# Optimization experiments

Hardware: AMD Instinct MI355X
Metric: run time of the kernel (lower is better)

## Reference

```python
import jax, jax.numpy as jnp
import numpy as np

N_NODES = 50000
N_EDGES = 800000
NFEAT, NHID, NCLASS = 512, 128, 16


def _with_self_loops(edge_idx, n):
    loop = jnp.arange(n, dtype=edge_idx.dtype)
    src = jnp.concatenate([edge_idx[0], loop])  # [E+N]
    dst = jnp.concatenate([edge_idx[1], loop])
    return src, dst


def gcn_conv(x, src, dst, W, b, n):
    # GCNConv with add aggregation, self-loops, symmetric normalization.
    h = x @ W  # [N, out]
    ones = jnp.ones(src.shape[0], dtype=h.dtype)
    deg = jax.ops.segment_sum(ones, dst, num_segments=n)  # in-degree incl. self-loops
    dinv = jnp.where(deg > 0, jax.lax.rsqrt(deg), 0.0)
    norm = dinv[src] * dinv[dst]  # [E+N]
    msg = h[src] * norm[:, None]  # gather + scale
    out = jax.ops.segment_sum(msg, dst, num_segments=n)  # scatter-add
    return out + b


def setup_inputs() -> dict:
    key = jax.random.key(0)
    ks = jax.random.split(key, 8)
    x = jax.random.normal(ks[0], (N_NODES, NFEAT), dtype=jnp.float32)
    edge_idx = jax.random.randint(ks[1], (2, N_EDGES), 0, N_NODES, dtype=jnp.int64)
    s1 = 1.0 / np.sqrt(NFEAT)
    s2 = 1.0 / np.sqrt(NHID)
    W1 = jax.random.uniform(ks[2], (NFEAT, NHID), jnp.float32, -s1, s1)
    b1 = jnp.zeros((NHID,), jnp.float32)
    W2 = jax.random.uniform(ks[3], (NHID, NHID), jnp.float32, -s2, s2)
    b2 = jnp.zeros((NHID,), jnp.float32)
    Wc = jax.random.uniform(ks[4], (NHID, NCLASS), jnp.float32, -s2, s2)
    bc = jax.random.uniform(ks[5], (NCLASS,), jnp.float32, -s2, s2)
    return {"x": x, "edge_idx": edge_idx, "W1": W1, "b1": b1, "W2": W2, "b2": b2, "Wc": Wc, "bc": bc}


def reference(x, edge_idx, W1, b1, W2, b2, Wc, bc):
    n = x.shape[0]
    src, dst = _with_self_loops(edge_idx, n)
    h = gcn_conv(x, src, dst, W1, b1, n)
    h = jax.nn.relu(h)  # dropout is identity in eval mode
    h = gcn_conv(h, src, dst, W2, b2, n)
    h = jax.nn.relu(h)
    logits = h @ Wc + bc
    return jax.nn.log_softmax(logits, axis=1)
```

## Files before the change

### kernel.cpp

```cpp
#include <hip/hip_runtime.h>
#include <math.h>

#define NFEAT 512
#define NHID  128
#define NCLASS 16
#define SCAN_BS 512

typedef __attribute__((ext_vector_type(8))) short short8;
typedef __attribute__((ext_vector_type(4))) float f32x4;

static __device__ __forceinline__ ushort f2b(float f) {
    union { float f; uint u; } v; v.f = f;
    uint r = v.u + 0x7FFFu + ((v.u >> 16) & 1u);
    return (ushort)(r >> 16);
}
static __device__ __forceinline__ float b2f(uint bits) {
    union { uint u; float f; } v; v.u = bits << 16; return v.f;
}


__global__ void k_init_deg(int* __restrict__ deg, int n) {
    int i = blockIdx.x * blockDim.x + threadIdx.x;
    if (i < n) deg[i] = 1;
}

__global__ void k_count(const int* __restrict__ dst, int e, int* __restrict__ deg) {
    int i = blockIdx.x * blockDim.x + threadIdx.x;
    if (i < e) atomicAdd(&deg[dst[i]], 1);
}

__global__ void k_dinv(const int* __restrict__ deg, float* __restrict__ dinv,
                       int* __restrict__ cursor, int n) {
    int i = blockIdx.x * blockDim.x + threadIdx.x;
    if (i < n) {
        dinv[i] = rsqrtf((float)deg[i]);
        cursor[i] = 0;
    }
}

__global__ void k_scan1(const int* __restrict__ deg, int* __restrict__ offs,
                        int* __restrict__ bsum, int n) {
    __shared__ int s[SCAN_BS];
    int t = threadIdx.x;
    int i = blockIdx.x * SCAN_BS + t;
    int v = (i < n) ? deg[i] : 0;
    s[t] = v;
    for (int off = 1; off < SCAN_BS; off <<= 1) {
        __syncthreads();
        int x = (t >= off) ? s[t - off] : 0;
        __syncthreads();
        s[t] += x;
    }
    __syncthreads();
    if (i < n) offs[i] = s[t] - v;
    if (t == SCAN_BS - 1) bsum[blockIdx.x] = s[t];
}

__global__ void k_scan2(int* __restrict__ bsum, int* __restrict__ offs, int nb, int n) {
    if (threadIdx.x == 0 && blockIdx.x == 0) {
        int run = 0;
        for (int b = 0; b < nb; b++) { int x = bsum[b]; bsum[b] = run; run += x; }
        offs[n] = run;
    }
}

__global__ void k_scan3(int* __restrict__ offs, const int* __restrict__ bsum, int n) {
    int i = blockIdx.x * SCAN_BS + threadIdx.x;
    if (i < n) offs[i] += bsum[blockIdx.x];
}

__global__ void k_fill_edges(const int* __restrict__ src, const int* __restrict__ dst, int e,
                             const int* __restrict__ offs, int* __restrict__ cursor,
                             int* __restrict__ col) {
    int i = blockIdx.x * blockDim.x + threadIdx.x;
    if (i < e) {
        int d = dst[i];
        int p = atomicAdd(&cursor[d], 1);
        col[offs[d] + p] = src[i];
    }
}

__global__ void k_fill_self(const int* __restrict__ offs, int* __restrict__ cursor,
                            int* __restrict__ col, int n) {
    int i = blockIdx.x * blockDim.x + threadIdx.x;
    if (i < n) {
        int p = atomicAdd(&cursor[i], 1);
        col[offs[i] + p] = i;
    }
}


__global__ void k_tcast(const float* __restrict__ W, ushort* __restrict__ WT, int K) {
    int idx = blockIdx.x * 256 + threadIdx.x;
    if (idx < K * 128) {
        int k = idx >> 7, c = idx & 127;
        WT[(size_t)c * K + k] = f2b(W[idx]);
    }
}


template<int A_F32>
__global__ __launch_bounds__(256) void k_gemm(const void* __restrict__ Aptr,
                                              const ushort* __restrict__ WT,
                                              const float* __restrict__ rowscale,
                                              ushort* __restrict__ H, int M, int K) {
    __shared__ ushort As[128][40];
    __shared__ ushort Bs[128][40];

    const int tid = threadIdx.x;
    const int wid = tid >> 6, lane = tid & 63;
    const int wr = wid >> 1, wc = wid & 1;
    const int lr = lane & 15, lk = (lane >> 4) * 8;
    const int rowbase = blockIdx.x * 128;

    f32x4 acc[4][4];
#pragma unroll
    for (int i = 0; i < 4; i++)
#pragma unroll
        for (int j = 0; j < 4; j++) acc[i][j] = (f32x4)0.f;

    const int sr = tid >> 1;
    const int sh = (tid & 1) * 16;

    for (int k0 = 0; k0 < K; k0 += 32) {
        {
            int gr = rowbase + sr;
            ushort tmp[16];
            if (A_F32) {
                const float* A = (const float*)Aptr;
                if (gr < M) {
                    const float* p = A + (size_t)gr * K + k0 + sh;
#pragma unroll
                    for (int q = 0; q < 4; q++) {
                        float4 v = *(const float4*)(p + q * 4);
                        tmp[q * 4 + 0] = f2b(v.x); tmp[q * 4 + 1] = f2b(v.y);
                        tmp[q * 4 + 2] = f2b(v.z); tmp[q * 4 + 3] = f2b(v.w);
                    }
                } else {
#pragma unroll
                    for (int q = 0; q < 16; q++) tmp[q] = 0;
                }
            } else {
                const ushort* A = (const ushort*)Aptr;
                if (gr < M) {
                    const ushort* p = A + (size_t)gr * K + k0 + sh;
                    *(short8*)&tmp[0] = *(const short8*)(p);
                    *(short8*)&tmp[8] = *(const short8*)(p + 8);
                } else {
#pragma unroll
                    for (int q = 0; q < 16; q++) tmp[q] = 0;
                }
            }
            *(short8*)&As[sr][sh]     = *(short8*)&tmp[0];
            *(short8*)&As[sr][sh + 8] = *(short8*)&tmp[8];
        }
        {
#pragma unroll
            for (int t = 0; t < 2; t++) {
                int c = tid + t * 256;
                int row = c >> 2, q = c & 3;
                short8 v = *(const short8*)(WT + (size_t)row * K + k0 + q * 8);
                *(short8*)&Bs[row][q * 8] = v;
            }
        }
        __syncthreads();

        short8 af[4], bfv[4];
#pragma unroll
        for (int i = 0; i < 4; i++) af[i] = *(const short8*)&As[wr * 64 + i * 16 + lr][lk];
#pragma unroll
        for (int j = 0; j < 4; j++) bfv[j] = *(const short8*)&Bs[wc * 64 + j * 16 + lr][lk];
#pragma unroll
        for (int i = 0; i < 4; i++)
#pragma unroll
            for (int j = 0; j < 4; j++)
                acc[i][j] = __builtin_amdgcn_mfma_f32_16x16x32_bf16(af[i], bfv[j], acc[i][j], 0, 0, 0);
        __syncthreads();
    }

#pragma unroll
    for (int i = 0; i < 4; i++) {
#pragma unroll
        for (int r = 0; r < 4; r++) {
            int row = rowbase + wr * 64 + i * 16 + (lane >> 4) * 4 + r;
            if (row < M) {
                float sc = rowscale[row];
#pragma unroll
                for (int j = 0; j < 4; j++) {
                    int colg = wc * 64 + j * 16 + lr;
                    H[(size_t)row * 128 + colg] = f2b(acc[i][j][r] * sc);
                }
            }
        }
    }
}


template<int OUT_BF16>
__global__ __launch_bounds__(256) void k_agg(const ushort* __restrict__ h,
                                             const int* __restrict__ offs,
                                             const int* __restrict__ col,
                                             const float* __restrict__ dinv,
                                             const float* __restrict__ bias,
                                             void* __restrict__ outp, int n) {
    int wid = threadIdx.x >> 6, lane = threadIdx.x & 63;
    int v = blockIdx.x * 4 + wid;
    if (v >= n) return;
    int e0 = offs[v], e1 = offs[v + 1];
    int lx = lane * 2;
    float a0 = 0.f, a1 = 0.f;
    for (int base = e0; base < e1; base += 64) {
        int cnt = e1 - base; if (cnt > 64) cnt = 64;
        int myc = 0;
        if (base + lane < e1) myc = col[base + lane];
        int j = 0;
        for (; j + 8 <= cnt; j += 8) {
            uint pk[8];
#pragma unroll
            for (int q = 0; q < 8; q++) {
                int s = __shfl(myc, j + q);
                pk[q] = *(const uint*)(h + (size_t)s * 128 + lx);
            }
#pragma unroll
            for (int q = 0; q < 8; q++) {
                a0 += b2f(pk[q] & 0xffffu);
                a1 += b2f(pk[q] >> 16);
            }
        }
        for (; j < cnt; j++) {
            int s = __shfl(myc, j);
            uint p0 = *(const uint*)(h + (size_t)s * 128 + lx);
            a0 += b2f(p0 & 0xffffu);
            a1 += b2f(p0 >> 16);
        }
    }
    float dvv = dinv[v];
    float r0 = fmaxf(fmaf(a0, dvv, bias[lx + 0]), 0.f);
    float r1 = fmaxf(fmaf(a1, dvv, bias[lx + 1]), 0.f);
    if (OUT_BF16) {
        uint pk = (uint)f2b(r0) | ((uint)f2b(r1) << 16);
        *(uint*)((ushort*)outp + (size_t)v * 128 + lx) = pk;
    } else {
        *(float2*)((float*)outp + (size_t)v * 128 + lx) = make_float2(r0, r1);
    }
}


__global__ __launch_bounds__(256) void k_classify(const float* __restrict__ h,
                                                  const float* __restrict__ Wc,
                                                  const float* __restrict__ bc,
                                                  float* __restrict__ out, int n) {
    __shared__ float Ws[128 * 16];
    int tid = threadIdx.x;
#pragma unroll
    for (int t = 0; t < 8; t++) Ws[tid + 256 * t] = Wc[tid + 256 * t];
    __syncthreads();

    int g = tid >> 4;
    int j = tid & 15;
    int v = blockIdx.x * 16 + g;
    if (v >= n) return;

    float acc = bc[j];
    const float* hv = h + (size_t)v * 128;
    for (int k = 0; k < 128; k++) acc = fmaf(hv[k], Ws[k * 16 + j], acc);

    float m = acc;
#pragma unroll
    for (int o = 8; o >= 1; o >>= 1) m = fmaxf(m, __shfl_xor(m, o, 16));
    float s = expf(acc - m);
#pragma unroll
    for (int o = 8; o >= 1; o >>= 1) s += __shfl_xor(s, o, 16);
    out[(size_t)v * 16 + j] = acc - m - logf(s);
}


extern "C" void kernel_launch(void* const* d_in, const int* in_sizes, int n_in,
                              void* d_out, int out_size, void* d_ws, size_t ws_size,
                              hipStream_t stream) {
    const float* x  = (const float*)d_in[0];
    const int* eidx = (const int*)d_in[1];
    const float* W1 = (const float*)d_in[2];
    const float* b1 = (const float*)d_in[3];
    const float* W2 = (const float*)d_in[4];
    const float* b2 = (const float*)d_in[5];
    const float* Wc = (const float*)d_in[6];
    const float* bc = (const float*)d_in[7];
    float* out = (float*)d_out;

    const int N = in_sizes[0] / NFEAT;
    const int E = in_sizes[1] / 2;
    const int* src = eidx;
    const int* dst = eidx + E;

    char* p = (char*)d_ws;
    auto alloc = [&](size_t bytes) { char* r = p; p += (bytes + 255) & ~(size_t)255; return r; };
    int*    deg    = (int*)   alloc((size_t)N * 4);
    float*  dinv   = (float*) alloc((size_t)N * 4);
    int*    offs   = (int*)   alloc((size_t)(N + 1) * 4);
    int*    cursor = (int*)   alloc((size_t)N * 4);
    int*    col    = (int*)   alloc((size_t)(E + N) * 4);
    int*    bsum   = (int*)   alloc((size_t)256 * 4);
    ushort* W1T    = (ushort*)alloc((size_t)128 * NFEAT * 2);
    ushort* W2T    = (ushort*)alloc((size_t)128 * NHID * 2);
    ushort* bufA   = (ushort*)alloc((size_t)N * NHID * 2);
    float*  bufB   = (float*) alloc((size_t)N * NHID * 4);
    ushort* g1b    = (ushort*)bufB;

    const int nb = (N + SCAN_BS - 1) / SCAN_BS;

    k_init_deg<<<(N + 255) / 256, 256, 0, stream>>>(deg, N);
    k_count<<<(E + 255) / 256, 256, 0, stream>>>(dst, E, deg);
    k_dinv<<<(N + 255) / 256, 256, 0, stream>>>(deg, dinv, cursor, N);
    k_scan1<<<nb, SCAN_BS, 0, stream>>>(deg, offs, bsum, N);
    k_scan2<<<1, 64, 0, stream>>>(bsum, offs, nb, N);
    k_scan3<<<nb, SCAN_BS, 0, stream>>>(offs, bsum, N);
    k_fill_edges<<<(E + 255) / 256, 256, 0, stream>>>(src, dst, E, offs, cursor, col);
    k_fill_self<<<(N + 255) / 256, 256, 0, stream>>>(offs, cursor, col, N);

    k_tcast<<<(NFEAT * 128 + 255) / 256, 256, 0, stream>>>(W1, W1T, NFEAT);
    k_tcast<<<(NHID * 128 + 255) / 256, 256, 0, stream>>>(W2, W2T, NHID);

    const int gblocks = (N + 127) / 128;
    k_gemm<1><<<gblocks, 256, 0, stream>>>(x, W1T, dinv, bufA, N, NFEAT);
    k_agg<1><<<(N + 3) / 4, 256, 0, stream>>>(bufA, offs, col, dinv, b1, g1b, N);
    k_gemm<0><<<gblocks, 256, 0, stream>>>(g1b, W2T, dinv, bufA, N, NHID);
    k_agg<0><<<(N + 3) / 4, 256, 0, stream>>>(bufA, offs, col, dinv, b2, bufB, N);
    k_classify<<<(N + 15) / 16, 256, 0, stream>>>(bufB, Wc, bc, out, N);
}
```

Before: 241.2 us.

## Fuse second aggregation with classifier and log-softmax; widen gather batching

```diff
diff --git a/kernel.cpp b/kernel.cpp
--- a/kernel.cpp
+++ b/kernel.cpp
@@ -196,82 +196,108 @@
 }
 
 
-template<int OUT_BF16>
+template<int B>
+static __device__ __forceinline__ void gbatch(const ushort* __restrict__ h, int lx, int myc,
+                                              int j, float& a0, float& a1) {
+    uint pk[B];
+#pragma unroll
+    for (int q = 0; q < B; q++) {
+        int s = __shfl(myc, j + q);
+        pk[q] = *(const uint*)(h + (size_t)s * 128 + lx);
+    }
+#pragma unroll
+    for (int q = 0; q < B; q++) {
+        a0 += b2f(pk[q] & 0xffffu);
+        a1 += b2f(pk[q] >> 16);
+    }
+}
+
+static __device__ __forceinline__ void gather_node(const ushort* __restrict__ h, int lx,
+                                                   const int* __restrict__ col, int lane,
+                                                   int e0, int e1, float& a0, float& a1) {
+    for (int base = e0; base < e1; base += 64) {
+        int cnt = e1 - base; if (cnt > 64) cnt = 64;
+        int myc = (base + lane < e1) ? col[base + lane] : 0;
+        int j = 0;
+        while (j + 32 <= cnt) { gbatch<32>(h, lx, myc, j, a0, a1); j += 32; }
+        if (j + 16 <= cnt) { gbatch<16>(h, lx, myc, j, a0, a1); j += 16; }
+        if (j + 8 <= cnt)  { gbatch<8>(h, lx, myc, j, a0, a1);  j += 8; }
+        if (j + 4 <= cnt)  { gbatch<4>(h, lx, myc, j, a0, a1);  j += 4; }
+        if (j + 2 <= cnt)  { gbatch<2>(h, lx, myc, j, a0, a1);  j += 2; }
+        if (j < cnt)       { gbatch<1>(h, lx, myc, j, a0, a1); }
+    }
+}
+
+
 __global__ __launch_bounds__(256) void k_agg(const ushort* __restrict__ h,
                                              const int* __restrict__ offs,
                                              const int* __restrict__ col,
                                              const float* __restrict__ dinv,
                                              const float* __restrict__ bias,
-                                             void* __restrict__ outp, int n) {
+                                             ushort* __restrict__ outp, int n) {
     int wid = threadIdx.x >> 6, lane = threadIdx.x & 63;
     int v = blockIdx.x * 4 + wid;
     if (v >= n) return;
     int e0 = offs[v], e1 = offs[v + 1];
     int lx = lane * 2;
     float a0 = 0.f, a1 = 0.f;
-    for (int base = e0; base < e1; base += 64) {
-        int cnt = e1 - base; if (cnt > 64) cnt = 64;
-        int myc = 0;
-        if (base + lane < e1) myc = col[base + lane];
-        int j = 0;
-        for (; j + 8 <= cnt; j += 8) {
-            uint pk[8];
-#pragma unroll
-            for (int q = 0; q < 8; q++) {
-                int s = __shfl(myc, j + q);
-                pk[q] = *(const uint*)(h + (size_t)s * 128 + lx);
-            }
-#pragma unroll
-            for (int q = 0; q < 8; q++) {
-                a0 += b2f(pk[q] & 0xffffu);
-                a1 += b2f(pk[q] >> 16);
-            }
-        }
-        for (; j < cnt; j++) {
-            int s = __shfl(myc, j);
-            uint p0 = *(const uint*)(h + (size_t)s * 128 + lx);
-            a0 += b2f(p0 & 0xffffu);
-            a1 += b2f(p0 >> 16);
-        }
-    }
+    gather_node(h, lx, col, lane, e0, e1, a0, a1);
     float dvv = dinv[v];
     float r0 = fmaxf(fmaf(a0, dvv, bias[lx + 0]), 0.f);
     float r1 = fmaxf(fmaf(a1, dvv, bias[lx + 1]), 0.f);
-    if (OUT_BF16) {
-        uint pk = (uint)f2b(r0) | ((uint)f2b(r1) << 16);
-        *(uint*)((ushort*)outp + (size_t)v * 128 + lx) = pk;
-    } else {
-        *(float2*)((float*)outp + (size_t)v * 128 + lx) = make_float2(r0, r1);
-    }
-}
-
-
-__global__ __launch_bounds__(256) void k_classify(const float* __restrict__ h,
-                                                  const float* __restrict__ Wc,
-                                                  const float* __restrict__ bc,
-                                                  float* __restrict__ out, int n) {
+    uint pk = (uint)f2b(r0) | ((uint)f2b(r1) << 16);
+    *(uint*)(outp + (size_t)v * 128 + lx) = pk;
+}
+
+
+__global__ __launch_bounds__(256) void k_agg_cls(const ushort* __restrict__ h,
+                                                 const int* __restrict__ offs,
+                                                 const int* __restrict__ col,
+                                                 const float* __restrict__ dinv,
+                                                 const float* __restrict__ bias,
+                                                 const float* __restrict__ Wc,
+                                                 const float* __restrict__ bc,
+                                                 float* __restrict__ out, int n) {
     __shared__ float Ws[128 * 16];
+    __shared__ float shh[4][128];
     int tid = threadIdx.x;
 #pragma unroll
     for (int t = 0; t < 8; t++) Ws[tid + 256 * t] = Wc[tid + 256 * t];
     __syncthreads();
 
-    int g = tid >> 4;
-    int j = tid & 15;
-    int v = blockIdx.x * 16 + g;
-    if (v >= n) return;
-
-    float acc = bc[j];
-    const float* hv = h + (size_t)v * 128;
-    for (int k = 0; k < 128; k++) acc = fmaf(hv[k], Ws[k * 16 + j], acc);
+    int wid = tid >> 6, lane = tid & 63;
+    int v = blockIdx.x * 4 + wid;
+    bool valid = v < n;
+    int e0 = 0, e1 = 0;
+    if (valid) { e0 = offs[v]; e1 = offs[v + 1]; }
+    int lx = lane * 2;
+    float a0 = 0.f, a1 = 0.f;
+    gather_node(h, lx, col, lane, e0, e1, a0, a1);
+    float dvv = valid ? dinv[v] : 0.f;
+    float r0 = fmaxf(fmaf(a0, dvv, bias[lx + 0]), 0.f);
+    float r1 = fmaxf(fmaf(a1, dvv, bias[lx + 1]), 0.f);
+    shh[wid][lx] = r0;
+    shh[wid][lx + 1] = r1;
+    __syncthreads();
+
+    int j = lane & 15, c = lane >> 4;
+    float acc = 0.f;
+#pragma unroll
+    for (int f0 = 0; f0 < 32; f0++) {
+        int f = c * 32 + f0;
+        acc = fmaf(shh[wid][f], Ws[f * 16 + j], acc);
+    }
+    acc += __shfl_xor(acc, 16);
+    acc += __shfl_xor(acc, 32);
+    acc += bc[j];
 
     float m = acc;
 #pragma unroll
-    for (int o = 8; o >= 1; o >>= 1) m = fmaxf(m, __shfl_xor(m, o, 16));
+    for (int o = 8; o >= 1; o >>= 1) m = fmaxf(m, __shfl_xor(m, o));
     float s = expf(acc - m);
 #pragma unroll
-    for (int o = 8; o >= 1; o >>= 1) s += __shfl_xor(s, o, 16);
-    out[(size_t)v * 16 + j] = acc - m - logf(s);
+    for (int o = 8; o >= 1; o >>= 1) s += __shfl_xor(s, o);
+    if (valid && lane < 16) out[(size_t)v * 16 + j] = acc - m - logf(s);
 }
 
 
@@ -304,8 +330,7 @@
     ushort* W1T    = (ushort*)alloc((size_t)128 * NFEAT * 2);
     ushort* W2T    = (ushort*)alloc((size_t)128 * NHID * 2);
     ushort* bufA   = (ushort*)alloc((size_t)N * NHID * 2);
-    float*  bufB   = (float*) alloc((size_t)N * NHID * 4);
-    ushort* g1b    = (ushort*)bufB;
+    ushort* g1b    = (ushort*)alloc((size_t)N * NHID * 2);
 
     const int nb = (N + SCAN_BS - 1) / SCAN_BS;
 
@@ -323,8 +348,7 @@
 
     const int gblocks = (N + 127) / 128;
     k_gemm<1><<<gblocks, 256, 0, stream>>>(x, W1T, dinv, bufA, N, NFEAT);
-    k_agg<1><<<(N + 3) / 4, 256, 0, stream>>>(bufA, offs, col, dinv, b1, g1b, N);
+    k_agg<<<(N + 3) / 4, 256, 0, stream>>>(bufA, offs, col, dinv, b1, g1b, N);
     k_gemm<0><<<gblocks, 256, 0, stream>>>(g1b, W2T, dinv, bufA, N, NHID);
-    k_agg<0><<<(N + 3) / 4, 256, 0, stream>>>(bufA, offs, col, dinv, b2, bufB, N);
-    k_classify<<<(N + 15) / 16, 256, 0, stream>>>(bufB, Wc, bc, out, N);
-}
+    k_agg_cls<<<(N + 3) / 4, 256, 0, stream>>>(bufA, offs, col, dinv, b2, Wc, bc, out, N);
+}
```

Measured after the change: 241.4 us. Within noise of the previous version (+0.1%).
